# Kernel optimization log

Measured on AMD Instinct MI355X. Metric: run time of the kernel, lower is better.

The kernel has to match this reference:

```python
import jax, jax.numpy as jnp
import numpy as np

N_NODES = 50000
N_EDGES = 800000
N_GRAPHS = 512
F_IN = 96
HID = 128


def gcn_conv(x, src, dst, W, b, n_nodes):
    # PyG GCNConv: add self-loops, symmetric normalization, scatter-add aggregation.
    h = x @ W  # [N, H] transform first (cheaper than per-edge transform)
    # in-degree from edges (weight 1) plus the self-loop
    deg = jax.ops.segment_sum(jnp.ones_like(dst, dtype=h.dtype), dst,
                              num_segments=n_nodes) + 1.0  # [N]
    dinv = jax.lax.rsqrt(deg)  # D^{-1/2}
    norm = dinv[src] * dinv[dst]  # [E] edge norm
    msg = h[src] * norm[:, None]  # [E, H] gather + scale
    agg = jax.ops.segment_sum(msg, dst, num_segments=n_nodes)  # scatter-add
    agg = agg + h * (1.0 / deg)[:, None]  # self-loop contribution (norm = 1/deg)
    return agg + b


def global_mean_pool(x, batch, num_graphs):
    sums = jax.ops.segment_sum(x, batch, num_segments=num_graphs)  # [G, H]
    cnt = jax.ops.segment_sum(jnp.ones((x.shape[0],), x.dtype), batch,
                              num_segments=num_graphs)  # [G]
    return sums / jnp.maximum(cnt, 1.0)[:, None]


def setup_inputs() -> dict:
    key = jax.random.key(0)
    ks = jax.random.split(key, 8)
    x = jax.random.normal(ks[0], (N_NODES, F_IN), dtype=jnp.float32)
    edge_index = jax.random.randint(ks[1], (2, N_EDGES), 0, N_NODES, dtype=jnp.int64)
    batch = jnp.sort(jax.random.randint(ks[2], (N_NODES,), 0, N_GRAPHS, dtype=jnp.int64))
    W1 = jax.random.normal(ks[3], (F_IN, HID), dtype=jnp.float32) * (1.0 / np.sqrt(F_IN))
    b1 = jnp.zeros((HID,), jnp.float32)
    W2 = jax.random.normal(ks[4], (HID, HID), dtype=jnp.float32) * (1.0 / np.sqrt(HID))
    b2 = jnp.zeros((HID,), jnp.float32)
    Wlin = jax.random.normal(ks[5], (HID, 2), dtype=jnp.float32) * (1.0 / np.sqrt(HID))
    blin = jnp.zeros((2,), jnp.float32)
    return {"x": x, "edge_index": edge_index, "batch": batch, "num_graphs": N_GRAPHS,
            "W1": W1, "b1": b1, "W2": W2, "b2": b2, "Wlin": Wlin, "blin": blin}


def reference(x, edge_index, batch, num_graphs, W1, b1, W2, b2, Wlin, blin):
    src, dst = edge_index[0], edge_index[1]
    n = x.shape[0]
    h = jax.nn.relu(gcn_conv(x, src, dst, W1, b1, n))
    h = jax.nn.relu(gcn_conv(h, src, dst, W2, b2, n))
    g = global_mean_pool(h, batch, num_graphs)  # [G, H]
    # dropout(p=0.2) is identity in eval mode
    return g @ Wlin + blin  # [G, 2]
```

## Files before the change

kernel.cpp:

```cpp
#include <hip/hip_runtime.h>

#define N_NODES 50000
#define N_PAD   50048
#define N_EDGES 800000
#define N_GRAPHS 512
#define F_IN 96
#define HID 128
#define NBUCK 196
#define CHUNK 4096
#define NCH   196
#define NB_G 782

typedef __bf16 bf16x8 __attribute__((ext_vector_type(8)));
typedef float  f32x4  __attribute__((ext_vector_type(4)));

__device__ __forceinline__ unsigned short f2bf(float f) {
    union { float f; unsigned u; } v; v.f = f;
    unsigned r = v.u + 0x7FFFu + ((v.u >> 16) & 1u);
    return (unsigned short)(r >> 16);
}
__device__ __forceinline__ float bflo(unsigned u) {
    union { unsigned u; float f; } v; v.u = u << 16; return v.f;
}
__device__ __forceinline__ float bfhi(unsigned u) {
    union { unsigned u; float f; } v; v.u = u & 0xFFFF0000u; return v.f;
}

__device__ __forceinline__ uint4 frag_of(const float* __restrict__ W, int KS, int idx) {
    int t = idx / (KS * 64);
    int rem = idx % (KS * 64);
    int s = rem / 64;
    int l = rem & 63;
    int n = t * 16 + (l & 15);
    int k0 = s * 32 + (l >> 4) * 8;
    unsigned short v[8];
#pragma unroll
    for (int j = 0; j < 8; ++j) v[j] = f2bf(W[(long)(k0 + j) * 128 + n]);
    uint4 o;
    o.x = (unsigned)v[0] | ((unsigned)v[1] << 16);
    o.y = (unsigned)v[2] | ((unsigned)v[3] << 16);
    o.z = (unsigned)v[4] | ((unsigned)v[5] << 16);
    o.w = (unsigned)v[6] | ((unsigned)v[7] << 16);
    return o;
}

__global__ __launch_bounds__(256) void k1_fused(const int* __restrict__ dst,
                                                const float* __restrict__ W1,
                                                const float* __restrict__ W2,
                                                unsigned short* __restrict__ W2f,
                                                int* __restrict__ bh,
                                                const float* __restrict__ x,
                                                unsigned short* __restrict__ hp) {
    __shared__ uint4 w1lds[1536];
    int blk = blockIdx.x;
    int tid = threadIdx.x;

    if (blk < NB_G) {
        for (int idx = tid; idx < 1536; idx += 256) w1lds[idx] = frag_of(W1, 3, idx);
        __syncthreads();

        const int KS = 3;
        const int wave = tid >> 6, lane = tid & 63;
        const int r0 = blk * 64 + wave * 16;
        f32x4 acc[8];
#pragma unroll
        for (int t = 0; t < 8; ++t) acc[t] = (f32x4){0.f, 0.f, 0.f, 0.f};
        int arow = r0 + (lane & 15);
        if (arow >= N_NODES) arow = N_NODES - 1;
        const int kq = (lane >> 4) * 8;
        for (int s = 0; s < KS; ++s) {
            const float* ap = x + (long)arow * F_IN + s * 32 + kq;
            float4 a0 = *(const float4*)(ap);
            float4 a1 = *(const float4*)(ap + 4);
            union { uint4 u; bf16x8 b; } af;
            af.u.x = (unsigned)f2bf(a0.x) | ((unsigned)f2bf(a0.y) << 16);
            af.u.y = (unsigned)f2bf(a0.z) | ((unsigned)f2bf(a0.w) << 16);
            af.u.z = (unsigned)f2bf(a1.x) | ((unsigned)f2bf(a1.y) << 16);
            af.u.w = (unsigned)f2bf(a1.z) | ((unsigned)f2bf(a1.w) << 16);
#pragma unroll
            for (int t = 0; t < 8; ++t) {
                union { uint4 u; bf16x8 b; } bfr;
                bfr.u = w1lds[(t * KS + s) * 64 + lane];
                acc[t] = __builtin_amdgcn_mfma_f32_16x16x32_bf16(af.b, bfr.b, acc[t], 0, 0, 0);
            }
        }
        const int q = lane >> 4;
#pragma unroll
        for (int t = 0; t < 8; ++t) {
            int col = t * 16 + (lane & 15);
#pragma unroll
            for (int r = 0; r < 4; ++r) {
                int row = r0 + q * 4 + r;
                if (row < N_NODES) hp[(long)row * 128 + col] = f2bf(acc[t][r]);
            }
        }
    } else if (blk < NB_G + NCH) {
        int* bhist = (int*)w1lds;
        int c = blk - NB_G;
        for (int i = tid; i < NBUCK; i += 256) bhist[i] = 0;
        __syncthreads();
        int e0 = c * CHUNK, e1 = min(e0 + CHUNK, N_EDGES);
        int n4 = (e1 - e0) >> 2;
        const uint4* d4 = (const uint4*)(dst + e0);
        for (int i = tid; i < n4; i += 256) {
            uint4 d = d4[i];
            atomicAdd(&bhist[d.x >> 8], 1);
            atomicAdd(&bhist[d.y >> 8], 1);
            atomicAdd(&bhist[d.z >> 8], 1);
            atomicAdd(&bhist[d.w >> 8], 1);
        }
        __syncthreads();
        for (int i = tid; i < NBUCK; i += 256) bh[c * NBUCK + i] = bhist[i];
    } else {
        int idx = (blk - NB_G - NCH) * 256 + tid;
        *(uint4*)(W2f + (long)idx * 8) = frag_of(W2, 4, idx);
    }
}

__global__ __launch_bounds__(256) void goff_scan(const int* __restrict__ bh,
                                                 int* __restrict__ goff,
                                                 int* __restrict__ total) {
    __shared__ int s[256];
    int b = blockIdx.x;
    int c = threadIdx.x;
    int v = (c < NCH) ? bh[c * NBUCK + b] : 0;
    s[c] = v;
    __syncthreads();
#pragma unroll
    for (int off = 1; off < 256; off <<= 1) {
        int t = 0;
        if (c >= off) t = s[c - off];
        __syncthreads();
        if (c >= off) s[c] += t;
        __syncthreads();
    }
    if (c < NCH) goff[c * NBUCK + b] = s[c] - v;
    if (c == 255) total[b] = s[255];
}

__global__ __launch_bounds__(256) void scatter_pairs(const int* __restrict__ src,
                                                     const int* __restrict__ dst,
                                                     const int* __restrict__ goff,
                                                     const int* __restrict__ total,
                                                     unsigned* __restrict__ ebuf) {
    __shared__ int ts[256];
    __shared__ int lgoff[NBUCK];
    __shared__ int lcur[NBUCK];
    int tid = threadIdx.x;
    int c = blockIdx.x;
    int tv = (tid < NBUCK) ? total[tid] : 0;
    ts[tid] = tv;
    __syncthreads();
#pragma unroll
    for (int off = 1; off < 256; off <<= 1) {
        int t = 0;
        if (tid >= off) t = ts[tid - off];
        __syncthreads();
        if (tid >= off) ts[tid] += t;
        __syncthreads();
    }
    if (tid < NBUCK) {
        lgoff[tid] = goff[c * NBUCK + tid] + (ts[tid] - tv);
        lcur[tid] = 0;
    }
    __syncthreads();
    int e0 = c * CHUNK, e1 = min(e0 + CHUNK, N_EDGES);
    for (int e = e0 + tid; e < e1; e += 256) {
        int d = dst[e];
        int b = d >> 8;
        int slot = atomicAdd(&lcur[b], 1);
        ebuf[lgoff[b] + slot] = (unsigned)src[e] | ((unsigned)(d & 255) << 16);
    }
}

__global__ __launch_bounds__(256) void bucket_sort(const unsigned* __restrict__ ebuf,
                                                   const int* __restrict__ total,
                                                   int* __restrict__ rowstart,
                                                   int* __restrict__ cnt,
                                                   float* __restrict__ dinv,
                                                   int* __restrict__ esrc) {
    __shared__ int ts[256];
    __shared__ int lcnt[256];
    __shared__ int ssc[256];
    __shared__ int ncur[256];
    int b = blockIdx.x, tid = threadIdx.x;
    int tv = (tid < NBUCK) ? total[tid] : 0;
    ts[tid] = tv;
    __syncthreads();
#pragma unroll
    for (int off = 1; off < 256; off <<= 1) {
        int t = 0;
        if (tid >= off) t = ts[tid - off];
        __syncthreads();
        if (tid >= off) ts[tid] += t;
        __syncthreads();
    }
    int r1 = ts[b];
    int r0 = r1 - total[b];
    int nbase = b * 256;
    lcnt[tid] = 0;
    __syncthreads();
    for (int i = r0 + tid; i < r1; i += 256)
        atomicAdd(&lcnt[ebuf[i] >> 16], 1);
    __syncthreads();
    int c = lcnt[tid];
    ssc[tid] = c;
    __syncthreads();
#pragma unroll
    for (int off = 1; off < 256; off <<= 1) {
        int t = 0;
        if (tid >= off) t = ssc[tid - off];
        __syncthreads();
        if (tid >= off) ssc[tid] += t;
        __syncthreads();
    }
    int rs = r0 + ssc[tid] - c;
    ncur[tid] = rs;
    int node = nbase + tid;
    if (node < N_NODES) {
        rowstart[node] = rs;
        cnt[node] = c;
        dinv[node] = rsqrtf((float)c + 1.0f);
    }
    __syncthreads();
    for (int i = r0 + tid; i < r1; i += 256) {
        unsigned p = ebuf[i];
        int pos = atomicAdd(&ncur[p >> 16], 1);
        esrc[pos] = (int)(p & 0xFFFFu);
    }
}

#define H1_STRIDE 17
__global__ __launch_bounds__(256) void agg1_gemm2(const uint4* __restrict__ hp4,
                                                  const int* __restrict__ esrc,
                                                  const int* __restrict__ rowstart,
                                                  const int* __restrict__ cnt,
                                                  const float* __restrict__ dinv,
                                                  const float* __restrict__ b1,
                                                  const unsigned short* __restrict__ W2f,
                                                  unsigned short* __restrict__ hp2) {
    __shared__ uint4 h1[16 * H1_STRIDE];
    const int tid = threadIdx.x;
    const int wave = tid >> 6, lane = tid & 63;
    const int eslot = lane >> 4, ug = lane & 15;
    const int nbase = blockIdx.x * 16;

    for (int i = 0; i < 4; ++i) {
        int node = nbase + wave * 4 + i;
        int start = rowstart[node];
        int end = start + cnt[node];

        float a[8];
#pragma unroll
        for (int k = 0; k < 8; ++k) a[k] = 0.f;

        for (int j = start; j < end; j += 16) {
            int e[4];
            uint4 v[4];
            float w[4];
#pragma unroll
            for (int q = 0; q < 4; ++q) {
                e[q] = j + q * 4 + eslot;
                int s = esrc[min(e[q], end - 1)];
                v[q] = hp4[(long)s * 16 + ug];
                w[q] = dinv[s];
            }
#pragma unroll
            for (int q = 0; q < 4; ++q) {
                if (e[q] < end) {
                    a[0] += w[q] * bflo(v[q].x); a[1] += w[q] * bfhi(v[q].x);
                    a[2] += w[q] * bflo(v[q].y); a[3] += w[q] * bfhi(v[q].y);
                    a[4] += w[q] * bflo(v[q].z); a[5] += w[q] * bfhi(v[q].z);
                    a[6] += w[q] * bflo(v[q].w); a[7] += w[q] * bfhi(v[q].w);
                }
            }
        }

#pragma unroll
        for (int k = 0; k < 8; ++k) {
            a[k] += __shfl_xor(a[k], 16);
            a[k] += __shfl_xor(a[k], 32);
        }

        if (eslot == 0) {
            float d = dinv[node];
            uint4 vs = hp4[(long)node * 16 + ug];
            a[0] += d * bflo(vs.x); a[1] += d * bfhi(vs.x);
            a[2] += d * bflo(vs.y); a[3] += d * bfhi(vs.y);
            a[4] += d * bflo(vs.z); a[5] += d * bfhi(vs.z);
            a[6] += d * bflo(vs.w); a[7] += d * bfhi(vs.w);
            float4 c0 = *(const float4*)(b1 + ug * 8);
            float4 c1 = *(const float4*)(b1 + ug * 8 + 4);
            float o0 = fmaxf(d * a[0] + c0.x, 0.f), o1 = fmaxf(d * a[1] + c0.y, 0.f);
            float o2 = fmaxf(d * a[2] + c0.z, 0.f), o3 = fmaxf(d * a[3] + c0.w, 0.f);
            float o4 = fmaxf(d * a[4] + c1.x, 0.f), o5 = fmaxf(d * a[5] + c1.y, 0.f);
            float o6 = fmaxf(d * a[6] + c1.z, 0.f), o7 = fmaxf(d * a[7] + c1.w, 0.f);
            uint4 o;
            o.x = (unsigned)f2bf(o0) | ((unsigned)f2bf(o1) << 16);
            o.y = (unsigned)f2bf(o2) | ((unsigned)f2bf(o3) << 16);
            o.z = (unsigned)f2bf(o4) | ((unsigned)f2bf(o5) << 16);
            o.w = (unsigned)f2bf(o6) | ((unsigned)f2bf(o7) << 16);
            h1[(wave * 4 + i) * H1_STRIDE + ug] = o;
        }
    }
    __syncthreads();

    const int KS = 4;
    f32x4 acc[2];
    acc[0] = (f32x4){0.f, 0.f, 0.f, 0.f};
    acc[1] = (f32x4){0.f, 0.f, 0.f, 0.f};
    const int m = lane & 15;
    for (int s = 0; s < KS; ++s) {
        union { uint4 u; bf16x8 b; } af;
        af.u = h1[m * H1_STRIDE + s * 4 + eslot];
#pragma unroll
        for (int tt = 0; tt < 2; ++tt) {
            int t = wave * 2 + tt;
            union { uint4 u; bf16x8 b; } bfr;
            bfr.u = *(const uint4*)(W2f + ((long)(t * KS + s) * 64 + lane) * 8);
            acc[tt] = __builtin_amdgcn_mfma_f32_16x16x32_bf16(af.b, bfr.b, acc[tt], 0, 0, 0);
        }
    }
    const int q = lane >> 4;
    float dv[4];
#pragma unroll
    for (int r = 0; r < 4; ++r) dv[r] = dinv[nbase + q * 4 + r];
#pragma unroll
    for (int tt = 0; tt < 2; ++tt) {
        int col = (wave * 2 + tt) * 16 + (lane & 15);
#pragma unroll
        for (int r = 0; r < 4; ++r) {
            int row = nbase + q * 4 + r;
            hp2[(long)row * 128 + col] = f2bf(acc[tt][r] * dv[r]);
        }
    }
}

__global__ __launch_bounds__(256) void aggregate4(const uint4* __restrict__ hp4,
                                                  const int* __restrict__ esrc,
                                                  const int* __restrict__ rowstart,
                                                  const int* __restrict__ cnt,
                                                  const float* __restrict__ dinv,
                                                  const float* __restrict__ bias,
                                                  uint4* __restrict__ hout4) {
    int node = blockIdx.x * 4 + (threadIdx.x >> 6);
    if (node >= N_NODES) return;
    int lane = threadIdx.x & 63;
    int eslot = lane >> 4;
    int ug = lane & 15;
    int start = rowstart[node];
    int end = start + cnt[node];

    float a[8];
#pragma unroll
    for (int k = 0; k < 8; ++k) a[k] = 0.f;

    for (int j = start; j < end; j += 16) {
        int e[4];
        uint4 v[4];
#pragma unroll
        for (int q = 0; q < 4; ++q) {
            e[q] = j + q * 4 + eslot;
            int s = esrc[min(e[q], end - 1)];
            v[q] = hp4[(long)s * 16 + ug];
        }
#pragma unroll
        for (int q = 0; q < 4; ++q) {
            if (e[q] < end) {
                a[0] += bflo(v[q].x); a[1] += bfhi(v[q].x);
                a[2] += bflo(v[q].y); a[3] += bfhi(v[q].y);
                a[4] += bflo(v[q].z); a[5] += bfhi(v[q].z);
                a[6] += bflo(v[q].w); a[7] += bfhi(v[q].w);
            }
        }
    }

#pragma unroll
    for (int k = 0; k < 8; ++k) {
        a[k] += __shfl_xor(a[k], 16);
        a[k] += __shfl_xor(a[k], 32);
    }

    if (eslot == 0) {
        uint4 vs = hp4[(long)node * 16 + ug];
        a[0] += bflo(vs.x); a[1] += bfhi(vs.x);
        a[2] += bflo(vs.y); a[3] += bfhi(vs.y);
        a[4] += bflo(vs.z); a[5] += bfhi(vs.z);
        a[6] += bflo(vs.w); a[7] += bfhi(vs.w);
        float d = dinv[node];
        float4 b0 = *(const float4*)(bias + ug * 8);
        float4 b1 = *(const float4*)(bias + ug * 8 + 4);
        float o0 = fmaxf(d * a[0] + b0.x, 0.f), o1 = fmaxf(d * a[1] + b0.y, 0.f);
        float o2 = fmaxf(d * a[2] + b0.z, 0.f), o3 = fmaxf(d * a[3] + b0.w, 0.f);
        float o4 = fmaxf(d * a[4] + b1.x, 0.f), o5 = fmaxf(d * a[5] + b1.y, 0.f);
        float o6 = fmaxf(d * a[6] + b1.z, 0.f), o7 = fmaxf(d * a[7] + b1.w, 0.f);
        uint4 o;
        o.x = (unsigned)f2bf(o0) | ((unsigned)f2bf(o1) << 16);
        o.y = (unsigned)f2bf(o2) | ((unsigned)f2bf(o3) << 16);
        o.z = (unsigned)f2bf(o4) | ((unsigned)f2bf(o5) << 16);
        o.w = (unsigned)f2bf(o6) | ((unsigned)f2bf(o7) << 16);
        hout4[(long)node * 16 + ug] = o;
    }
}

__global__ __launch_bounds__(128) void pool_head(const unsigned short* __restrict__ h,
                                                 const int* __restrict__ batch,
                                                 const float* __restrict__ Wlin,
                                                 const float* __restrict__ blin,
                                                 float* __restrict__ out) {
    __shared__ int bnd[2];
    int g = blockIdx.x;
    int c = threadIdx.x;
    if (c < 2) {
        int target = g + c;
        int lo = 0, hi = N_NODES;
        while (lo < hi) {
            int mid = (lo + hi) >> 1;
            if (batch[mid] < target) lo = mid + 1;
            else hi = mid;
        }
        bnd[c] = lo;
    }
    __syncthreads();
    int s = bnd[0], e = bnd[1];

    float sum = 0.f;
    for (int i = s; i < e; ++i) {
        union { unsigned u; float f; } v;
        v.u = (unsigned)h[(long)i * 128 + c] << 16;
        sum += v.f;
    }
    float inv = (e > s) ? 1.0f / (float)(e - s) : 1.0f;
    float m = sum * inv;

    __shared__ float red[128][2];
    red[c][0] = m * Wlin[c * 2 + 0];
    red[c][1] = m * Wlin[c * 2 + 1];
    __syncthreads();
#pragma unroll
    for (int off = 64; off > 0; off >>= 1) {
        if (c < off) {
            red[c][0] += red[c + off][0];
            red[c][1] += red[c + off][1];
        }
        __syncthreads();
    }
    if (c < 2) out[g * 2 + c] = red[0][c] + blin[c];
}

extern "C" void kernel_launch(void* const* d_in, const int* in_sizes, int n_in,
                              void* d_out, int out_size, void* d_ws, size_t ws_size,
                              hipStream_t stream) {
    const float* x    = (const float*)d_in[0];
    const int*   ei   = (const int*)d_in[1];
    const int*   batch= (const int*)d_in[2];
    const float* W1   = (const float*)d_in[4];
    const float* b1   = (const float*)d_in[5];
    const float* W2   = (const float*)d_in[6];
    const float* b2   = (const float*)d_in[7];
    const float* Wlin = (const float*)d_in[8];
    const float* blin = (const float*)d_in[9];
    float* out = (float*)d_out;

    const int* src = ei;
    const int* dst = ei + N_EDGES;

    char* ws = (char*)d_ws;
    const size_t KB = 1024;
    const size_t MB = 1048576;

    float*    dinv     = (float*)(ws);
    int*      cnt      = (int*)  (ws + 256 * KB);
    int*      rowstart = (int*)  (ws + 512 * KB);
    int*      total    = (int*)  (ws + 768 * KB);
    int*      bh       = (int*)  (ws + 832 * KB);
    int*      goff     = (int*)  (ws + 1 * MB);
    unsigned* ebuf     = (unsigned*)(ws + 2 * MB);
    int*      esrc     = (int*)  (ws + 9 * MB);
    unsigned short* W2f = (unsigned short*)(ws + 12 * MB + 576 * KB);
    unsigned short* hp  = (unsigned short*)(ws + 13 * MB);
    unsigned short* hp2 = (unsigned short*)(ws + 26 * MB);
    unsigned short* h   = (unsigned short*)(ws + 39 * MB);

    const int NB_AG = (N_NODES + 3) / 4;
    const int NB_F  = N_NODES / 16;

    k1_fused<<<NB_G + NCH + 8, 256, 0, stream>>>(dst, W1, W2, W2f, bh, x, hp);
    goff_scan<<<NBUCK, 256, 0, stream>>>(bh, goff, total);
    scatter_pairs<<<NCH, 256, 0, stream>>>(src, dst, goff, total, ebuf);
    bucket_sort<<<NBUCK, 256, 0, stream>>>(ebuf, total, rowstart, cnt, dinv, esrc);

    agg1_gemm2<<<NB_F, 256, 0, stream>>>((const uint4*)hp, esrc, rowstart, cnt, dinv, b1, W2f, hp2);

    aggregate4<<<NB_AG, 256, 0, stream>>>((const uint4*)hp2, esrc, rowstart, cnt, dinv, b2, (uint4*)h);

    pool_head<<<N_GRAPHS, 128, 0, stream>>>(h, batch, Wlin, blin, out);
}
```

Before: 232.4 us.

## Fold final linear head into second aggregation before pooling

Uses linearity of mean pooling and the final linear layer: each node's post-ReLU features are projected to 2 outputs inside the second aggregation kernel, and only a float2 per node is written. The pooling kernel then averages 2 floats per node instead of 128 bf16 features, with 256 threads striding over nodes instead of one sequential loop per feature. This removes the 12.8MB write and re-read of the final hidden features and the serial per-graph pooling loop, at the cost of a little extra arithmetic and shuffles in the aggregation epilogue and a different floating-point summation order.

```diff
diff --git a/kernel.cpp b/kernel.cpp
--- a/kernel.cpp
+++ b/kernel.cpp
@@ -336,13 +336,14 @@
     }
 }
 
-__global__ __launch_bounds__(256) void aggregate4(const uint4* __restrict__ hp4,
-                                                  const int* __restrict__ esrc,
-                                                  const int* __restrict__ rowstart,
-                                                  const int* __restrict__ cnt,
-                                                  const float* __restrict__ dinv,
-                                                  const float* __restrict__ bias,
-                                                  uint4* __restrict__ hout4) {
+__global__ __launch_bounds__(256) void agg2_head(const uint4* __restrict__ hp4,
+                                                 const int* __restrict__ esrc,
+                                                 const int* __restrict__ rowstart,
+                                                 const int* __restrict__ cnt,
+                                                 const float* __restrict__ dinv,
+                                                 const float* __restrict__ bias,
+                                                 const float* __restrict__ Wlin,
+                                                 float2* __restrict__ nodeS) {
     int node = blockIdx.x * 4 + (threadIdx.x >> 6);
     if (node >= N_NODES) return;
     int lane = threadIdx.x & 63;
@@ -390,62 +391,61 @@
         float d = dinv[node];
         float4 b0 = *(const float4*)(bias + ug * 8);
         float4 b1 = *(const float4*)(bias + ug * 8 + 4);
-        float o0 = fmaxf(d * a[0] + b0.x, 0.f), o1 = fmaxf(d * a[1] + b0.y, 0.f);
-        float o2 = fmaxf(d * a[2] + b0.z, 0.f), o3 = fmaxf(d * a[3] + b0.w, 0.f);
-        float o4 = fmaxf(d * a[4] + b1.x, 0.f), o5 = fmaxf(d * a[5] + b1.y, 0.f);
-        float o6 = fmaxf(d * a[6] + b1.z, 0.f), o7 = fmaxf(d * a[7] + b1.w, 0.f);
-        uint4 o;
-        o.x = (unsigned)f2bf(o0) | ((unsigned)f2bf(o1) << 16);
-        o.y = (unsigned)f2bf(o2) | ((unsigned)f2bf(o3) << 16);
-        o.z = (unsigned)f2bf(o4) | ((unsigned)f2bf(o5) << 16);
-        o.w = (unsigned)f2bf(o6) | ((unsigned)f2bf(o7) << 16);
-        hout4[(long)node * 16 + ug] = o;
-    }
-}
-
-__global__ __launch_bounds__(128) void pool_head(const unsigned short* __restrict__ h,
-                                                 const int* __restrict__ batch,
-                                                 const float* __restrict__ Wlin,
-                                                 const float* __restrict__ blin,
-                                                 float* __restrict__ out) {
+        float o[8];
+        o[0] = fmaxf(d * a[0] + b0.x, 0.f); o[1] = fmaxf(d * a[1] + b0.y, 0.f);
+        o[2] = fmaxf(d * a[2] + b0.z, 0.f); o[3] = fmaxf(d * a[3] + b0.w, 0.f);
+        o[4] = fmaxf(d * a[4] + b1.x, 0.f); o[5] = fmaxf(d * a[5] + b1.y, 0.f);
+        o[6] = fmaxf(d * a[6] + b1.z, 0.f); o[7] = fmaxf(d * a[7] + b1.w, 0.f);
+#pragma unroll
+        for (int k = 0; k < 8; ++k) o[k] = bflo((unsigned)f2bf(o[k]));
+        const float4* wl = (const float4*)(Wlin + ug * 16);
+        float4 wA = wl[0], wB = wl[1], wC = wl[2], wD = wl[3];
+        float s0 = o[0]*wA.x + o[1]*wA.z + o[2]*wB.x + o[3]*wB.z
+                 + o[4]*wC.x + o[5]*wC.z + o[6]*wD.x + o[7]*wD.z;
+        float s1 = o[0]*wA.y + o[1]*wA.w + o[2]*wB.y + o[3]*wB.w
+                 + o[4]*wC.y + o[5]*wC.w + o[6]*wD.y + o[7]*wD.w;
+        s0 += __shfl_xor(s0, 1); s1 += __shfl_xor(s1, 1);
+        s0 += __shfl_xor(s0, 2); s1 += __shfl_xor(s1, 2);
+        s0 += __shfl_xor(s0, 4); s1 += __shfl_xor(s1, 4);
+        s0 += __shfl_xor(s0, 8); s1 += __shfl_xor(s1, 8);
+        if (ug == 0) nodeS[node] = make_float2(s0, s1);
+    }
+}
+
+__global__ __launch_bounds__(256) void pool_small(const float* __restrict__ nodeSf,
+                                                  const int* __restrict__ batch,
+                                                  const float* __restrict__ blin,
+                                                  float* __restrict__ out) {
     __shared__ int bnd[2];
+    __shared__ float red[256];
     int g = blockIdx.x;
-    int c = threadIdx.x;
-    if (c < 2) {
-        int target = g + c;
+    int t = threadIdx.x;
+    if (t < 2) {
+        int target = g + t;
         int lo = 0, hi = N_NODES;
         while (lo < hi) {
             int mid = (lo + hi) >> 1;
             if (batch[mid] < target) lo = mid + 1;
             else hi = mid;
         }
-        bnd[c] = lo;
+        bnd[t] = lo;
     }
     __syncthreads();
     int s = bnd[0], e = bnd[1];
-
+    int c = t & 1, i0 = t >> 1;
     float sum = 0.f;
-    for (int i = s; i < e; ++i) {
-        union { unsigned u; float f; } v;
-        v.u = (unsigned)h[(long)i * 128 + c] << 16;
-        sum += v.f;
-    }
-    float inv = (e > s) ? 1.0f / (float)(e - s) : 1.0f;
-    float m = sum * inv;
-
-    __shared__ float red[128][2];
-    red[c][0] = m * Wlin[c * 2 + 0];
-    red[c][1] = m * Wlin[c * 2 + 1];
-    __syncthreads();
-#pragma unroll
-    for (int off = 64; off > 0; off >>= 1) {
-        if (c < off) {
-            red[c][0] += red[c + off][0];
-            red[c][1] += red[c + off][1];
-        }
-        __syncthreads();
-    }
-    if (c < 2) out[g * 2 + c] = red[0][c] + blin[c];
+    for (int i = s + i0; i < e; i += 128) sum += nodeSf[i * 2 + c];
+    red[t] = sum;
+    __syncthreads();
+#pragma unroll
+    for (int off = 128; off >= 2; off >>= 1) {
+        if (t < off) red[t] += red[t + off];
+        __syncthreads();
+    }
+    if (t < 2) {
+        float inv = (e > s) ? 1.0f / (float)(e - s) : 1.0f;
+        out[g * 2 + t] = red[t] * inv + blin[t];
+    }
 }
 
 extern "C" void kernel_launch(void* const* d_in, const int* in_sizes, int n_in,
@@ -480,7 +480,7 @@
     unsigned short* W2f = (unsigned short*)(ws + 12 * MB + 576 * KB);
     unsigned short* hp  = (unsigned short*)(ws + 13 * MB);
     unsigned short* hp2 = (unsigned short*)(ws + 26 * MB);
-    unsigned short* h   = (unsigned short*)(ws + 39 * MB);
+    float2*   nodeS    = (float2*)(ws + 39 * MB);
 
     const int NB_AG = (N_NODES + 3) / 4;
     const int NB_F  = N_NODES / 16;
@@ -492,7 +492,7 @@
 
     agg1_gemm2<<<NB_F, 256, 0, stream>>>((const uint4*)hp, esrc, rowstart, cnt, dinv, b1, W2f, hp2);
 
-    aggregate4<<<NB_AG, 256, 0, stream>>>((const uint4*)hp2, esrc, rowstart, cnt, dinv, b2, (uint4*)h);
-
-    pool_head<<<N_GRAPHS, 128, 0, stream>>>(h, batch, Wlin, blin, out);
-}
+    agg2_head<<<NB_AG, 256, 0, stream>>>((const uint4*)hp2, esrc, rowstart, cnt, dinv, b2, Wlin, nodeS);
+
+    pool_small<<<N_GRAPHS, 256, 0, stream>>>((const float*)nodeS, batch, blin, out);
+}
```

Result: faster. 200.9 us (-13.6%).
